# Kernel optimization log

Hardware: AMD Instinct MI355X
Metric: run time of the kernel (lower is better)

Reference implementation:

```python
import jax, jax.numpy as jnp
import numpy as np

HIDDEN = 4096
INTER = 11008
GROUP = 128
B, S = 1, 2048


def setup_inputs() -> dict:
    key = jax.random.key(0)
    ks = jax.random.split(key, 10)
    inp = {
        "x": jax.random.normal(ks[0], (B, S, HIDDEN), dtype=jnp.float32),
        "gate_qw": jax.random.randint(ks[1], (INTER, HIDDEN), 0, 16, dtype=jnp.int32),
        "gate_qz": jax.random.randint(ks[2], (INTER, HIDDEN // GROUP), 0, 16, dtype=jnp.int32),
        "gate_scale": jax.random.uniform(ks[3], (INTER, HIDDEN // GROUP), dtype=jnp.float32) * 0.02,
        "gate_bias": jnp.zeros((INTER,), dtype=jnp.float32),
        "up_qw": jax.random.randint(ks[4], (INTER, HIDDEN), 0, 16, dtype=jnp.int32),
        "up_qz": jax.random.randint(ks[5], (INTER, HIDDEN // GROUP), 0, 16, dtype=jnp.int32),
        "up_scale": jax.random.uniform(ks[6], (INTER, HIDDEN // GROUP), dtype=jnp.float32) * 0.02,
        "up_bias": jnp.zeros((INTER,), dtype=jnp.float32),
        "down_qw": jax.random.randint(ks[7], (HIDDEN, INTER), 0, 16, dtype=jnp.int32),
        "down_qz": jax.random.randint(ks[8], (HIDDEN, INTER // GROUP), 0, 16, dtype=jnp.int32),
        "down_scale": jax.random.uniform(ks[9], (HIDDEN, INTER // GROUP), dtype=jnp.float32) * 0.02,
        "down_bias": jnp.zeros((HIDDEN,), dtype=jnp.float32),
        "group_size": GROUP,
    }
    return inp


def _dequant(qw, qz, scale, group_size):
    # qw: [O, I] int codes in [0,16); qz, scale: [O, I//g]
    O, I = qw.shape
    g = group_size
    q = qw.reshape(O, I // g, g).astype(jnp.float32)
    w = (q - qz[:, :, None].astype(jnp.float32)) * scale[:, :, None]
    return w.reshape(O, I)  # [O, I]


def reference(x, gate_qw, gate_qz, gate_scale, gate_bias,
              up_qw, up_qz, up_scale, up_bias,
              down_qw, down_qz, down_scale, down_bias, group_size):
    Wg = _dequant(gate_qw, gate_qz, gate_scale, group_size)   # [INTER, HIDDEN]
    Wu = _dequant(up_qw, up_qz, up_scale, group_size)         # [INTER, HIDDEN]
    Wd = _dequant(down_qw, down_qz, down_scale, group_size)   # [HIDDEN, INTER]
    g = jnp.einsum('bsh,ih->bsi', x, Wg) + gate_bias          # [B,S,INTER]
    u = jnp.einsum('bsh,ih->bsi', x, Wu) + up_bias            # [B,S,INTER]
    h = jax.nn.silu(g) * u                                    # SwiGLU
    y = jnp.einsum('bsi,hi->bsh', h, Wd) + down_bias          # [B,S,HIDDEN]
    return y
```

## Files before the change

### kernel.cpp

```cpp
#include <hip/hip_runtime.h>
#include <hip/hip_bf16.h>
#include <stdint.h>

#define SEQ    2048
#define HIDDEN 4096
#define INTER  11008

typedef short bf16x8 __attribute__((ext_vector_type(8)));
typedef float f32x4  __attribute__((ext_vector_type(4)));
typedef unsigned short u16x8 __attribute__((ext_vector_type(8)));

#define BAR()  asm volatile("s_barrier" ::: "memory")
#define WAIT6  asm volatile("s_waitcnt vmcnt(6)" ::: "memory")
#define WAIT4  asm volatile("s_waitcnt vmcnt(4)" ::: "memory")
#define WAIT0  asm volatile("s_waitcnt vmcnt(0)" ::: "memory")

__device__ __forceinline__ unsigned short f2bf(float f) {
    union { __hip_bfloat16 h; unsigned short u; } v;
    v.h = __float2bfloat16(f);
    return v.u;
}

__device__ __forceinline__ void gload_lds16(const void* g, void* lds) {
    __builtin_amdgcn_global_load_lds(
        (const __attribute__((address_space(1))) uint32_t*)g,
        (__attribute__((address_space(3))) uint32_t*)lds,
        16, 0, 0);
}

__global__ __launch_bounds__(256) void k_cvt_x(const float* __restrict__ x,
                                               unsigned short* __restrict__ xb) {
    int i = (blockIdx.x * 256 + threadIdx.x) * 4;
    float4 v = *(const float4*)(x + i);
    ushort4 o;
    o.x = f2bf(v.x); o.y = f2bf(v.y); o.z = f2bf(v.z); o.w = f2bf(v.w);
    *(ushort4*)(xb + i) = o;
}

__global__ __launch_bounds__(256) void k_dequant(
    const int* __restrict__ qw, const int* __restrict__ qz,
    const float* __restrict__ sc, unsigned short* __restrict__ w)
{
    size_t i = ((size_t)blockIdx.x * 256 + threadIdx.x) * 8;
    int gi = (int)(i >> 7);
    int   z = qz[gi];
    float s = sc[gi];
    float zs = -(float)z * s;
    int4 q0 = *(const int4*)(qw + i);
    int4 q1 = *(const int4*)(qw + i + 4);
    u16x8 o;
    o[0] = f2bf(fmaf((float)q0.x, s, zs));
    o[1] = f2bf(fmaf((float)q0.y, s, zs));
    o[2] = f2bf(fmaf((float)q0.z, s, zs));
    o[3] = f2bf(fmaf((float)q0.w, s, zs));
    o[4] = f2bf(fmaf((float)q1.x, s, zs));
    o[5] = f2bf(fmaf((float)q1.y, s, zs));
    o[6] = f2bf(fmaf((float)q1.z, s, zs));
    o[7] = f2bf(fmaf((float)q1.w, s, zs));
    *(u16x8*)(w + i) = o;
}

__global__ __launch_bounds__(512) void k_gate_up(
    const unsigned short* __restrict__ xb,
    const unsigned short* __restrict__ wg,
    const unsigned short* __restrict__ wu,
    const float* __restrict__ gbias, const float* __restrict__ ubias,
    unsigned short* __restrict__ h)
{
    __shared__ __align__(16) unsigned short A0[128 * 64], A1[128 * 64];
    __shared__ __align__(16) unsigned short Bg0[128 * 64], Bg1[128 * 64];
    __shared__ __align__(16) unsigned short Bu0[128 * 64], Bu1[128 * 64];

    const int orig = blockIdx.x;
    const int swz  = (orig & 7) * 172 + (orig >> 3);
    const int mt   = swz & 15;
    const int nt   = swz >> 4;
    const int m0   = mt * 128;
    const int n0   = nt * 128;

    const int t    = threadIdx.x;
    const int lane = t & 63;
    const int wave = t >> 6;
    const int wm = (wave >> 2) * 64;
    const int wn = (wave & 3) * 32;

    f32x4 accG[4][2], accU[4][2];
#pragma unroll
    for (int mi = 0; mi < 4; ++mi)
#pragma unroll
        for (int ni = 0; ni < 2; ++ni) {
            accG[mi][ni] = (f32x4){0.f, 0.f, 0.f, 0.f};
            accU[mi][ni] = (f32x4){0.f, 0.f, 0.f, 0.f};
        }

    auto stage = [&](unsigned short* At, unsigned short* Bgt, unsigned short* But,
                     int kt) {
        const int k0 = kt * 64;
#pragma unroll
        for (int cc = 0; cc < 2; ++cc) {
            int idx  = t + 512 * cc;
            int row  = idx >> 3;
            int scol = ((idx & 7) * 16) ^ ((row & 7) << 4);
            gload_lds16((const char*)(xb + (size_t)(m0 + row) * HIDDEN + k0) + scol,
                        (char*)At + idx * 16);
            gload_lds16((const char*)(wg + (size_t)(n0 + row) * HIDDEN + k0) + scol,
                        (char*)Bgt + idx * 16);
            gload_lds16((const char*)(wu + (size_t)(n0 + row) * HIDDEN + k0) + scol,
                        (char*)But + idx * 16);
        }
    };

    auto comp = [&](const unsigned short* At, const unsigned short* Bgt,
                    const unsigned short* But) {
#pragma unroll
        for (int kk = 0; kk < 2; ++kk) {
            bf16x8 af[4], bg[2], bu[2];
#pragma unroll
            for (int mi = 0; mi < 4; ++mi) {
                int row  = wm + mi * 16 + (lane & 15);
                int colb = kk * 64 + ((lane >> 4) * 16);
                af[mi] = *(const bf16x8*)((const char*)At + row * 128 +
                                          (colb ^ ((row & 7) << 4)));
            }
#pragma unroll
            for (int ni = 0; ni < 2; ++ni) {
                int row  = wn + ni * 16 + (lane & 15);
                int colb = kk * 64 + ((lane >> 4) * 16);
                int off  = row * 128 + (colb ^ ((row & 7) << 4));
                bg[ni] = *(const bf16x8*)((const char*)Bgt + off);
                bu[ni] = *(const bf16x8*)((const char*)But + off);
            }
            __builtin_amdgcn_s_setprio(1);
#pragma unroll
            for (int mi = 0; mi < 4; ++mi)
#pragma unroll
                for (int ni = 0; ni < 2; ++ni) {
                    accG[mi][ni] = __builtin_amdgcn_mfma_f32_16x16x32_bf16(
                        af[mi], bg[ni], accG[mi][ni], 0, 0, 0);
                    accU[mi][ni] = __builtin_amdgcn_mfma_f32_16x16x32_bf16(
                        af[mi], bu[ni], accU[mi][ni], 0, 0, 0);
                }
            __builtin_amdgcn_s_setprio(0);
        }
    };

    stage(A0, Bg0, Bu0, 0);
    for (int kt = 0; kt < 62; kt += 2) {
        stage(A1, Bg1, Bu1, kt + 1); WAIT6; BAR(); comp(A0, Bg0, Bu0); BAR();
        stage(A0, Bg0, Bu0, kt + 2); WAIT6; BAR(); comp(A1, Bg1, Bu1); BAR();
    }
    stage(A1, Bg1, Bu1, 63); WAIT6; BAR(); comp(A0, Bg0, Bu0); BAR();
    WAIT0; BAR(); comp(A1, Bg1, Bu1);

#pragma unroll
    for (int ni = 0; ni < 2; ++ni) {
        int col = n0 + wn + ni * 16 + (lane & 15);
        float gb = gbias[col], ub = ubias[col];
#pragma unroll
        for (int mi = 0; mi < 4; ++mi) {
#pragma unroll
            for (int j = 0; j < 4; ++j) {
                int row = m0 + wm + mi * 16 + ((lane >> 4) * 4) + j;
                float g = accG[mi][ni][j] + gb;
                float u = accU[mi][ni][j] + ub;
                float sig = 1.f / (1.f + __expf(-g));
                h[(size_t)row * INTER + col] = f2bf(g * sig * u);
            }
        }
    }
}

__global__ __launch_bounds__(512) void k_down(
    const unsigned short* __restrict__ h,
    const unsigned short* __restrict__ wd,
    const float* __restrict__ dbias,
    float* __restrict__ y)
{
    __shared__ __align__(16) unsigned short A0[128 * 64], A1[128 * 64];
    __shared__ __align__(16) unsigned short B0[128 * 64], B1[128 * 64];

    const int orig = blockIdx.x;
    const int swz  = (orig & 7) * 64 + (orig >> 3);
    const int mt   = swz & 15;
    const int nt   = swz >> 4;
    const int m0   = mt * 128;
    const int n0   = nt * 128;

    const int t    = threadIdx.x;
    const int lane = t & 63;
    const int wave = t >> 6;
    const int wm = (wave >> 2) * 64;
    const int wn = (wave & 3) * 32;

    f32x4 acc[4][2];
#pragma unroll
    for (int mi = 0; mi < 4; ++mi)
#pragma unroll
        for (int ni = 0; ni < 2; ++ni)
            acc[mi][ni] = (f32x4){0.f, 0.f, 0.f, 0.f};

    auto stage = [&](unsigned short* At, unsigned short* Bt, int kt) {
        const int k0 = kt * 64;
#pragma unroll
        for (int cc = 0; cc < 2; ++cc) {
            int idx  = t + 512 * cc;
            int row  = idx >> 3;
            int scol = ((idx & 7) * 16) ^ ((row & 7) << 4);
            gload_lds16((const char*)(h + (size_t)(m0 + row) * INTER + k0) + scol,
                        (char*)At + idx * 16);
            gload_lds16((const char*)(wd + (size_t)(n0 + row) * INTER + k0) + scol,
                        (char*)Bt + idx * 16);
        }
    };

    auto comp = [&](const unsigned short* At, const unsigned short* Bt) {
#pragma unroll
        for (int kk = 0; kk < 2; ++kk) {
            bf16x8 af[4], bd[2];
#pragma unroll
            for (int mi = 0; mi < 4; ++mi) {
                int row  = wm + mi * 16 + (lane & 15);
                int colb = kk * 64 + ((lane >> 4) * 16);
                af[mi] = *(const bf16x8*)((const char*)At + row * 128 +
                                          (colb ^ ((row & 7) << 4)));
            }
#pragma unroll
            for (int ni = 0; ni < 2; ++ni) {
                int row  = wn + ni * 16 + (lane & 15);
                int colb = kk * 64 + ((lane >> 4) * 16);
                bd[ni] = *(const bf16x8*)((const char*)Bt + row * 128 +
                                          (colb ^ ((row & 7) << 4)));
            }
            __builtin_amdgcn_s_setprio(1);
#pragma unroll
            for (int mi = 0; mi < 4; ++mi)
#pragma unroll
                for (int ni = 0; ni < 2; ++ni)
                    acc[mi][ni] = __builtin_amdgcn_mfma_f32_16x16x32_bf16(
                        af[mi], bd[ni], acc[mi][ni], 0, 0, 0);
            __builtin_amdgcn_s_setprio(0);
        }
    };

    stage(A0, B0, 0);
    for (int kt = 0; kt < 170; kt += 2) {
        stage(A1, B1, kt + 1); WAIT4; BAR(); comp(A0, B0); BAR();
        stage(A0, B0, kt + 2); WAIT4; BAR(); comp(A1, B1); BAR();
    }
    stage(A1, B1, 171); WAIT4; BAR(); comp(A0, B0); BAR();
    WAIT0; BAR(); comp(A1, B1);

#pragma unroll
    for (int ni = 0; ni < 2; ++ni) {
        int col = n0 + wn + ni * 16 + (lane & 15);
        float db = dbias[col];
#pragma unroll
        for (int mi = 0; mi < 4; ++mi) {
#pragma unroll
            for (int j = 0; j < 4; ++j) {
                int row = m0 + wm + mi * 16 + ((lane >> 4) * 4) + j;
                y[(size_t)row * HIDDEN + col] = acc[mi][ni][j] + db;
            }
        }
    }
}

extern "C" void kernel_launch(void* const* d_in, const int* in_sizes, int n_in,
                              void* d_out, int out_size, void* d_ws, size_t ws_size,
                              hipStream_t stream) {
    const float* x    = (const float*)d_in[0];
    const int*   gqw  = (const int*)d_in[1];
    const int*   gqz  = (const int*)d_in[2];
    const float* gsc  = (const float*)d_in[3];
    const float* gbia = (const float*)d_in[4];
    const int*   uqw  = (const int*)d_in[5];
    const int*   uqz  = (const int*)d_in[6];
    const float* usc  = (const float*)d_in[7];
    const float* ubia = (const float*)d_in[8];
    const int*   dqw  = (const int*)d_in[9];
    const int*   dqz  = (const int*)d_in[10];
    const float* dsc  = (const float*)d_in[11];
    const float* dbia = (const float*)d_in[12];
    float* y = (float*)d_out;

    const size_t N_XB = (size_t)SEQ * HIDDEN;
    const size_t N_H  = (size_t)SEQ * INTER;
    const size_t N_W  = (size_t)INTER * HIDDEN;

    unsigned short* xb  = (unsigned short*)d_ws;
    unsigned short* hh  = xb + N_XB;
    unsigned short* wgb = hh + N_H;
    unsigned short* wub = wgb + N_W;
    unsigned short* wdb = wgb;

    const int dq_blocks = (int)(N_W / 2048);

    k_cvt_x<<<(SEQ * HIDDEN) / 1024, 256, 0, stream>>>(x, xb);
    k_dequant<<<dq_blocks, 256, 0, stream>>>(gqw, gqz, gsc, wgb);
    k_dequant<<<dq_blocks, 256, 0, stream>>>(uqw, uqz, usc, wub);
    k_gate_up<<<dim3(1376), 512, 0, stream>>>(xb, wgb, wub, gbia, ubia, hh);
    k_dequant<<<dq_blocks, 256, 0, stream>>>(dqw, dqz, dsc, wdb);
    k_down<<<dim3(512), 512, 0, stream>>>(hh, wdb, dbia, y);
}
```

Measured before the change: 848.8 us.

## Enlarge gate/up tile to 256x128, drop double buffering and block swizzle

The gate/up kernel moves from a 128x128 tile to a 256x128 tile with 64x64 per-wave subtiles and twice the accumulators, halving the grid. This cuts repeated weight loads per output. Both GEMM kernels lose their double-buffered LDS pipeline with explicit vmcnt waits and now use a single buffer with __syncthreads around each k-step, so loads no longer overlap compute. The L2-friendly block-index swizzle is also removed, and the larger accumulator set raises register pressure.

```diff
diff --git a/kernel.cpp b/kernel.cpp
--- a/kernel.cpp
+++ b/kernel.cpp
@@ -9,11 +9,6 @@
 typedef short bf16x8 __attribute__((ext_vector_type(8)));
 typedef float f32x4  __attribute__((ext_vector_type(4)));
 typedef unsigned short u16x8 __attribute__((ext_vector_type(8)));
-
-#define BAR()  asm volatile("s_barrier" ::: "memory")
-#define WAIT6  asm volatile("s_waitcnt vmcnt(6)" ::: "memory")
-#define WAIT4  asm volatile("s_waitcnt vmcnt(4)" ::: "memory")
-#define WAIT0  asm volatile("s_waitcnt vmcnt(0)" ::: "memory")
 
 __device__ __forceinline__ unsigned short f2bf(float f) {
     union { __hip_bfloat16 h; unsigned short u; } v;
@@ -67,74 +62,77 @@
     const float* __restrict__ gbias, const float* __restrict__ ubias,
     unsigned short* __restrict__ h)
 {
-    __shared__ __align__(16) unsigned short A0[128 * 64], A1[128 * 64];
-    __shared__ __align__(16) unsigned short Bg0[128 * 64], Bg1[128 * 64];
-    __shared__ __align__(16) unsigned short Bu0[128 * 64], Bu1[128 * 64];
-
-    const int orig = blockIdx.x;
-    const int swz  = (orig & 7) * 172 + (orig >> 3);
-    const int mt   = swz & 15;
-    const int nt   = swz >> 4;
-    const int m0   = mt * 128;
-    const int n0   = nt * 128;
+    __shared__ __align__(16) unsigned short At[256 * 64];
+    __shared__ __align__(16) unsigned short Bg[128 * 64];
+    __shared__ __align__(16) unsigned short Bu[128 * 64];
+
+    const int bid = blockIdx.x;
+    const int mt  = bid & 7;
+    const int nt  = bid >> 3;
+    const int m0  = mt * 256;
+    const int n0  = nt * 128;
 
     const int t    = threadIdx.x;
     const int lane = t & 63;
     const int wave = t >> 6;
-    const int wm = (wave >> 2) * 64;
-    const int wn = (wave & 3) * 32;
-
-    f32x4 accG[4][2], accU[4][2];
+    const int wm = (wave >> 1) * 64;
+    const int wn = (wave & 1) * 64;
+
+    f32x4 accG[4][4], accU[4][4];
 #pragma unroll
     for (int mi = 0; mi < 4; ++mi)
 #pragma unroll
-        for (int ni = 0; ni < 2; ++ni) {
+        for (int ni = 0; ni < 4; ++ni) {
             accG[mi][ni] = (f32x4){0.f, 0.f, 0.f, 0.f};
             accU[mi][ni] = (f32x4){0.f, 0.f, 0.f, 0.f};
         }
 
-    auto stage = [&](unsigned short* At, unsigned short* Bgt, unsigned short* But,
-                     int kt) {
+    for (int kt = 0; kt < HIDDEN / 64; ++kt) {
         const int k0 = kt * 64;
-#pragma unroll
-        for (int cc = 0; cc < 2; ++cc) {
+
+#pragma unroll
+        for (int cc = 0; cc < 4; ++cc) {
             int idx  = t + 512 * cc;
             int row  = idx >> 3;
             int scol = ((idx & 7) * 16) ^ ((row & 7) << 4);
             gload_lds16((const char*)(xb + (size_t)(m0 + row) * HIDDEN + k0) + scol,
                         (char*)At + idx * 16);
+        }
+#pragma unroll
+        for (int cc = 0; cc < 2; ++cc) {
+            int idx  = t + 512 * cc;
+            int row  = idx >> 3;
+            int scol = ((idx & 7) * 16) ^ ((row & 7) << 4);
             gload_lds16((const char*)(wg + (size_t)(n0 + row) * HIDDEN + k0) + scol,
-                        (char*)Bgt + idx * 16);
+                        (char*)Bg + idx * 16);
             gload_lds16((const char*)(wu + (size_t)(n0 + row) * HIDDEN + k0) + scol,
-                        (char*)But + idx * 16);
-        }
-    };
-
-    auto comp = [&](const unsigned short* At, const unsigned short* Bgt,
-                    const unsigned short* But) {
+                        (char*)Bu + idx * 16);
+        }
+
+        __syncthreads();
+
 #pragma unroll
         for (int kk = 0; kk < 2; ++kk) {
-            bf16x8 af[4], bg[2], bu[2];
+            bf16x8 af[4], bg[4], bu[4];
+            int colb = kk * 64 + ((lane >> 4) * 16);
 #pragma unroll
             for (int mi = 0; mi < 4; ++mi) {
-                int row  = wm + mi * 16 + (lane & 15);
-                int colb = kk * 64 + ((lane >> 4) * 16);
+                int row = wm + mi * 16 + (lane & 15);
                 af[mi] = *(const bf16x8*)((const char*)At + row * 128 +
                                           (colb ^ ((row & 7) << 4)));
             }
 #pragma unroll
-            for (int ni = 0; ni < 2; ++ni) {
-                int row  = wn + ni * 16 + (lane & 15);
-                int colb = kk * 64 + ((lane >> 4) * 16);
-                int off  = row * 128 + (colb ^ ((row & 7) << 4));
-                bg[ni] = *(const bf16x8*)((const char*)Bgt + off);
-                bu[ni] = *(const bf16x8*)((const char*)But + off);
+            for (int ni = 0; ni < 4; ++ni) {
+                int row = wn + ni * 16 + (lane & 15);
+                int off = row * 128 + (colb ^ ((row & 7) << 4));
+                bg[ni] = *(const bf16x8*)((const char*)Bg + off);
+                bu[ni] = *(const bf16x8*)((const char*)Bu + off);
             }
             __builtin_amdgcn_s_setprio(1);
 #pragma unroll
             for (int mi = 0; mi < 4; ++mi)
 #pragma unroll
-                for (int ni = 0; ni < 2; ++ni) {
+                for (int ni = 0; ni < 4; ++ni) {
                     accG[mi][ni] = __builtin_amdgcn_mfma_f32_16x16x32_bf16(
                         af[mi], bg[ni], accG[mi][ni], 0, 0, 0);
                     accU[mi][ni] = __builtin_amdgcn_mfma_f32_16x16x32_bf16(
@@ -142,18 +140,12 @@
                 }
             __builtin_amdgcn_s_setprio(0);
         }
-    };
-
-    stage(A0, Bg0, Bu0, 0);
-    for (int kt = 0; kt < 62; kt += 2) {
-        stage(A1, Bg1, Bu1, kt + 1); WAIT6; BAR(); comp(A0, Bg0, Bu0); BAR();
-        stage(A0, Bg0, Bu0, kt + 2); WAIT6; BAR(); comp(A1, Bg1, Bu1); BAR();
-    }
-    stage(A1, Bg1, Bu1, 63); WAIT6; BAR(); comp(A0, Bg0, Bu0); BAR();
-    WAIT0; BAR(); comp(A1, Bg1, Bu1);
-
-#pragma unroll
-    for (int ni = 0; ni < 2; ++ni) {
+
+        __syncthreads();
+    }
+
+#pragma unroll
+    for (int ni = 0; ni < 4; ++ni) {
         int col = n0 + wn + ni * 16 + (lane & 15);
         float gb = gbias[col], ub = ubias[col];
 #pragma unroll
@@ -176,15 +168,14 @@
     const float* __restrict__ dbias,
     float* __restrict__ y)
 {
-    __shared__ __align__(16) unsigned short A0[128 * 64], A1[128 * 64];
-    __shared__ __align__(16) unsigned short B0[128 * 64], B1[128 * 64];
-
-    const int orig = blockIdx.x;
-    const int swz  = (orig & 7) * 64 + (orig >> 3);
-    const int mt   = swz & 15;
-    const int nt   = swz >> 4;
-    const int m0   = mt * 128;
-    const int n0   = nt * 128;
+    __shared__ __align__(16) unsigned short At[128 * 64];
+    __shared__ __align__(16) unsigned short Bd[128 * 64];
+
+    const int bid = blockIdx.x;
+    const int mt  = bid & 15;
+    const int nt  = bid >> 4;
+    const int m0  = mt * 128;
+    const int n0  = nt * 128;
 
     const int t    = threadIdx.x;
     const int lane = t & 63;
@@ -199,8 +190,9 @@
         for (int ni = 0; ni < 2; ++ni)
             acc[mi][ni] = (f32x4){0.f, 0.f, 0.f, 0.f};
 
-    auto stage = [&](unsigned short* At, unsigned short* Bt, int kt) {
+    for (int kt = 0; kt < INTER / 64; ++kt) {
         const int k0 = kt * 64;
+
 #pragma unroll
         for (int cc = 0; cc < 2; ++cc) {
             int idx  = t + 512 * cc;
@@ -209,11 +201,11 @@
             gload_lds16((const char*)(h + (size_t)(m0 + row) * INTER + k0) + scol,
                         (char*)At + idx * 16);
             gload_lds16((const char*)(wd + (size_t)(n0 + row) * INTER + k0) + scol,
-                        (char*)Bt + idx * 16);
-        }
-    };
-
-    auto comp = [&](const unsigned short* At, const unsigned short* Bt) {
+                        (char*)Bd + idx * 16);
+        }
+
+        __syncthreads();
+
 #pragma unroll
         for (int kk = 0; kk < 2; ++kk) {
             bf16x8 af[4], bd[2];
@@ -228,7 +220,7 @@
             for (int ni = 0; ni < 2; ++ni) {
                 int row  = wn + ni * 16 + (lane & 15);
                 int colb = kk * 64 + ((lane >> 4) * 16);
-                bd[ni] = *(const bf16x8*)((const char*)Bt + row * 128 +
+                bd[ni] = *(const bf16x8*)((const char*)Bd + row * 128 +
                                           (colb ^ ((row & 7) << 4)));
             }
             __builtin_amdgcn_s_setprio(1);
@@ -240,15 +232,9 @@
                         af[mi], bd[ni], acc[mi][ni], 0, 0, 0);
             __builtin_amdgcn_s_setprio(0);
         }
-    };
-
-    stage(A0, B0, 0);
-    for (int kt = 0; kt < 170; kt += 2) {
-        stage(A1, B1, kt + 1); WAIT4; BAR(); comp(A0, B0); BAR();
-        stage(A0, B0, kt + 2); WAIT4; BAR(); comp(A1, B1); BAR();
-    }
-    stage(A1, B1, 171); WAIT4; BAR(); comp(A0, B0); BAR();
-    WAIT0; BAR(); comp(A1, B1);
+
+        __syncthreads();
+    }
 
 #pragma unroll
     for (int ni = 0; ni < 2; ++ni) {
@@ -298,7 +284,7 @@
     k_cvt_x<<<(SEQ * HIDDEN) / 1024, 256, 0, stream>>>(x, xb);
     k_dequant<<<dq_blocks, 256, 0, stream>>>(gqw, gqz, gsc, wgb);
     k_dequant<<<dq_blocks, 256, 0, stream>>>(uqw, uqz, usc, wub);
-    k_gate_up<<<dim3(1376), 512, 0, stream>>>(xb, wgb, wub, gbia, ubia, hh);
+    k_gate_up<<<dim3(688), 512, 0, stream>>>(xb, wgb, wub, gbia, ubia, hh);
     k_dequant<<<dq_blocks, 256, 0, stream>>>(dqw, dqz, dsc, wdb);
     k_down<<<dim3(512), 512, 0, stream>>>(hh, wdb, dbia, y);
 }
```

Result: no change. 845.9 us (-0.3%).

## Switch GEMM pipelines to triple-buffered 32-wide K stages with new LDS swizzle

Applied to the files above, without the earlier changes.

Both the gate/up and down GEMMs now stage 32-element K slices into three rotating LDS buffers instead of 64-element slices into two. Each thread issues one 16-byte direct-to-LDS load per operand per stage, using a new row-pair swizzle for the stores and a matching fragment read pattern. This keeps two stages of global loads in flight ahead of compute, and the total LDS footprint per block shrinks. The cost is twice as many barriers and wait points, with half as many MFMAs between each pair.

```diff
diff --git a/kernel.cpp b/kernel.cpp
--- a/kernel.cpp
+++ b/kernel.cpp
@@ -11,9 +11,11 @@
 typedef unsigned short u16x8 __attribute__((ext_vector_type(8)));
 
 #define BAR()  asm volatile("s_barrier" ::: "memory")
-#define WAIT6  asm volatile("s_waitcnt vmcnt(6)" ::: "memory")
-#define WAIT4  asm volatile("s_waitcnt vmcnt(4)" ::: "memory")
-#define WAIT0  asm volatile("s_waitcnt vmcnt(0)" ::: "memory")
+#define W6()   asm volatile("s_waitcnt vmcnt(6)" ::: "memory")
+#define W4()   asm volatile("s_waitcnt vmcnt(4)" ::: "memory")
+#define W3()   asm volatile("s_waitcnt vmcnt(3)" ::: "memory")
+#define W2()   asm volatile("s_waitcnt vmcnt(2)" ::: "memory")
+#define W0()   asm volatile("s_waitcnt vmcnt(0)" ::: "memory")
 
 __device__ __forceinline__ unsigned short f2bf(float f) {
     union { __hip_bfloat16 h; unsigned short u; } v;
@@ -60,6 +62,7 @@
     *(u16x8*)(w + i) = o;
 }
 
+
 __global__ __launch_bounds__(512) void k_gate_up(
     const unsigned short* __restrict__ xb,
     const unsigned short* __restrict__ wg,
@@ -67,9 +70,9 @@
     const float* __restrict__ gbias, const float* __restrict__ ubias,
     unsigned short* __restrict__ h)
 {
-    __shared__ __align__(16) unsigned short A0[128 * 64], A1[128 * 64];
-    __shared__ __align__(16) unsigned short Bg0[128 * 64], Bg1[128 * 64];
-    __shared__ __align__(16) unsigned short Bu0[128 * 64], Bu1[128 * 64];
+    __shared__ __align__(16) unsigned short A_[3][128 * 32];
+    __shared__ __align__(16) unsigned short Bg_[3][128 * 32];
+    __shared__ __align__(16) unsigned short Bu_[3][128 * 32];
 
     const int orig = blockIdx.x;
     const int swz  = (orig & 7) * 172 + (orig >> 3);
@@ -84,6 +87,14 @@
     const int wm = (wave >> 2) * 64;
     const int wn = (wave & 3) * 32;
 
+    const int srow = t >> 3;
+    const int sl   = (t & 7) ^ (srow & 7);
+    const int lrow = srow * 2 + (sl >> 2);
+    const int lcolb = (sl & 3) * 16;
+
+    const int sS   = ((((lane & 1) << 2) | (lane >> 4)) ^ ((lane >> 1) & 7)) * 16;
+    const int lrh  = (lane & 15) >> 1;
+
     f32x4 accG[4][2], accU[4][2];
 #pragma unroll
     for (int mi = 0; mi < 4; ++mi)
@@ -93,64 +104,50 @@
             accU[mi][ni] = (f32x4){0.f, 0.f, 0.f, 0.f};
         }
 
-    auto stage = [&](unsigned short* At, unsigned short* Bgt, unsigned short* But,
-                     int kt) {
-        const int k0 = kt * 64;
-#pragma unroll
-        for (int cc = 0; cc < 2; ++cc) {
-            int idx  = t + 512 * cc;
-            int row  = idx >> 3;
-            int scol = ((idx & 7) * 16) ^ ((row & 7) << 4);
-            gload_lds16((const char*)(xb + (size_t)(m0 + row) * HIDDEN + k0) + scol,
-                        (char*)At + idx * 16);
-            gload_lds16((const char*)(wg + (size_t)(n0 + row) * HIDDEN + k0) + scol,
-                        (char*)Bgt + idx * 16);
-            gload_lds16((const char*)(wu + (size_t)(n0 + row) * HIDDEN + k0) + scol,
-                        (char*)But + idx * 16);
-        }
-    };
-
-    auto comp = [&](const unsigned short* At, const unsigned short* Bgt,
-                    const unsigned short* But) {
-#pragma unroll
-        for (int kk = 0; kk < 2; ++kk) {
-            bf16x8 af[4], bg[2], bu[2];
-#pragma unroll
-            for (int mi = 0; mi < 4; ++mi) {
-                int row  = wm + mi * 16 + (lane & 15);
-                int colb = kk * 64 + ((lane >> 4) * 16);
-                af[mi] = *(const bf16x8*)((const char*)At + row * 128 +
-                                          (colb ^ ((row & 7) << 4)));
+    auto stage = [&](int buf, int ph) {
+        const int k0 = ph * 32;
+        const char* xs = (const char*)(xb + (size_t)(m0 + lrow) * HIDDEN + k0) + lcolb;
+        const char* gs = (const char*)(wg + (size_t)(n0 + lrow) * HIDDEN + k0) + lcolb;
+        const char* us = (const char*)(wu + (size_t)(n0 + lrow) * HIDDEN + k0) + lcolb;
+        gload_lds16(xs, (char*)A_[buf]  + t * 16);
+        gload_lds16(gs, (char*)Bg_[buf] + t * 16);
+        gload_lds16(us, (char*)Bu_[buf] + t * 16);
+    };
+
+    auto comp = [&](int buf) {
+        bf16x8 af[4], bg[2], bu[2];
+#pragma unroll
+        for (int mi = 0; mi < 4; ++mi)
+            af[mi] = *(const bf16x8*)((const char*)A_[buf] +
+                        (wm / 2 + mi * 8 + lrh) * 128 + sS);
+#pragma unroll
+        for (int ni = 0; ni < 2; ++ni) {
+            int off = (wn / 2 + ni * 8 + lrh) * 128 + sS;
+            bg[ni] = *(const bf16x8*)((const char*)Bg_[buf] + off);
+            bu[ni] = *(const bf16x8*)((const char*)Bu_[buf] + off);
+        }
+        __builtin_amdgcn_s_setprio(1);
+#pragma unroll
+        for (int mi = 0; mi < 4; ++mi)
+#pragma unroll
+            for (int ni = 0; ni < 2; ++ni) {
+                accG[mi][ni] = __builtin_amdgcn_mfma_f32_16x16x32_bf16(
+                    af[mi], bg[ni], accG[mi][ni], 0, 0, 0);
+                accU[mi][ni] = __builtin_amdgcn_mfma_f32_16x16x32_bf16(
+                    af[mi], bu[ni], accU[mi][ni], 0, 0, 0);
             }
-#pragma unroll
-            for (int ni = 0; ni < 2; ++ni) {
-                int row  = wn + ni * 16 + (lane & 15);
-                int colb = kk * 64 + ((lane >> 4) * 16);
-                int off  = row * 128 + (colb ^ ((row & 7) << 4));
-                bg[ni] = *(const bf16x8*)((const char*)Bgt + off);
-                bu[ni] = *(const bf16x8*)((const char*)But + off);
-            }
-            __builtin_amdgcn_s_setprio(1);
-#pragma unroll
-            for (int mi = 0; mi < 4; ++mi)
-#pragma unroll
-                for (int ni = 0; ni < 2; ++ni) {
-                    accG[mi][ni] = __builtin_amdgcn_mfma_f32_16x16x32_bf16(
-                        af[mi], bg[ni], accG[mi][ni], 0, 0, 0);
-                    accU[mi][ni] = __builtin_amdgcn_mfma_f32_16x16x32_bf16(
-                        af[mi], bu[ni], accU[mi][ni], 0, 0, 0);
-                }
-            __builtin_amdgcn_s_setprio(0);
-        }
-    };
-
-    stage(A0, Bg0, Bu0, 0);
-    for (int kt = 0; kt < 62; kt += 2) {
-        stage(A1, Bg1, Bu1, kt + 1); WAIT6; BAR(); comp(A0, Bg0, Bu0); BAR();
-        stage(A0, Bg0, Bu0, kt + 2); WAIT6; BAR(); comp(A1, Bg1, Bu1); BAR();
-    }
-    stage(A1, Bg1, Bu1, 63); WAIT6; BAR(); comp(A0, Bg0, Bu0); BAR();
-    WAIT0; BAR(); comp(A1, Bg1, Bu1);
+        __builtin_amdgcn_s_setprio(0);
+    };
+
+    stage(0, 0);
+    stage(1, 1);
+    for (int ph = 0; ph + 4 < 128; ph += 3) {
+        stage(2, ph + 2); W6(); BAR(); comp(0); BAR();
+        stage(0, ph + 3); W6(); BAR(); comp(1); BAR();
+        stage(1, ph + 4); W6(); BAR(); comp(2); BAR();
+    }
+    W3(); BAR(); comp(0);
+    W0(); BAR(); comp(1);
 
 #pragma unroll
     for (int ni = 0; ni < 2; ++ni) {
@@ -176,8 +173,8 @@
     const float* __restrict__ dbias,
     float* __restrict__ y)
 {
-    __shared__ __align__(16) unsigned short A0[128 * 64], A1[128 * 64];
-    __shared__ __align__(16) unsigned short B0[128 * 64], B1[128 * 64];
+    __shared__ __align__(16) unsigned short A_[3][128 * 32];
+    __shared__ __align__(16) unsigned short B_[3][128 * 32];
 
     const int orig = blockIdx.x;
     const int swz  = (orig & 7) * 64 + (orig >> 3);
@@ -192,6 +189,14 @@
     const int wm = (wave >> 2) * 64;
     const int wn = (wave & 3) * 32;
 
+    const int srow = t >> 3;
+    const int sl   = (t & 7) ^ (srow & 7);
+    const int lrow = srow * 2 + (sl >> 2);
+    const int lcolb = (sl & 3) * 16;
+
+    const int sS   = ((((lane & 1) << 2) | (lane >> 4)) ^ ((lane >> 1) & 7)) * 16;
+    const int lrh  = (lane & 15) >> 1;
+
     f32x4 acc[4][2];
 #pragma unroll
     for (int mi = 0; mi < 4; ++mi)
@@ -199,56 +204,43 @@
         for (int ni = 0; ni < 2; ++ni)
             acc[mi][ni] = (f32x4){0.f, 0.f, 0.f, 0.f};
 
-    auto stage = [&](unsigned short* At, unsigned short* Bt, int kt) {
-        const int k0 = kt * 64;
-#pragma unroll
-        for (int cc = 0; cc < 2; ++cc) {
-            int idx  = t + 512 * cc;
-            int row  = idx >> 3;
-            int scol = ((idx & 7) * 16) ^ ((row & 7) << 4);
-            gload_lds16((const char*)(h + (size_t)(m0 + row) * INTER + k0) + scol,
-                        (char*)At + idx * 16);
-            gload_lds16((const char*)(wd + (size_t)(n0 + row) * INTER + k0) + scol,
-                        (char*)Bt + idx * 16);
-        }
-    };
-
-    auto comp = [&](const unsigned short* At, const unsigned short* Bt) {
-#pragma unroll
-        for (int kk = 0; kk < 2; ++kk) {
-            bf16x8 af[4], bd[2];
-#pragma unroll
-            for (int mi = 0; mi < 4; ++mi) {
-                int row  = wm + mi * 16 + (lane & 15);
-                int colb = kk * 64 + ((lane >> 4) * 16);
-                af[mi] = *(const bf16x8*)((const char*)At + row * 128 +
-                                          (colb ^ ((row & 7) << 4)));
-            }
-#pragma unroll
-            for (int ni = 0; ni < 2; ++ni) {
-                int row  = wn + ni * 16 + (lane & 15);
-                int colb = kk * 64 + ((lane >> 4) * 16);
-                bd[ni] = *(const bf16x8*)((const char*)Bt + row * 128 +
-                                          (colb ^ ((row & 7) << 4)));
-            }
-            __builtin_amdgcn_s_setprio(1);
-#pragma unroll
-            for (int mi = 0; mi < 4; ++mi)
-#pragma unroll
-                for (int ni = 0; ni < 2; ++ni)
-                    acc[mi][ni] = __builtin_amdgcn_mfma_f32_16x16x32_bf16(
-                        af[mi], bd[ni], acc[mi][ni], 0, 0, 0);
-            __builtin_amdgcn_s_setprio(0);
-        }
-    };
-
-    stage(A0, B0, 0);
-    for (int kt = 0; kt < 170; kt += 2) {
-        stage(A1, B1, kt + 1); WAIT4; BAR(); comp(A0, B0); BAR();
-        stage(A0, B0, kt + 2); WAIT4; BAR(); comp(A1, B1); BAR();
-    }
-    stage(A1, B1, 171); WAIT4; BAR(); comp(A0, B0); BAR();
-    WAIT0; BAR(); comp(A1, B1);
+    auto stage = [&](int buf, int ph) {
+        const int k0 = ph * 32;
+        gload_lds16((const char*)(h  + (size_t)(m0 + lrow) * INTER + k0) + lcolb,
+                    (char*)A_[buf] + t * 16);
+        gload_lds16((const char*)(wd + (size_t)(n0 + lrow) * INTER + k0) + lcolb,
+                    (char*)B_[buf] + t * 16);
+    };
+
+    auto comp = [&](int buf) {
+        bf16x8 af[4], bd[2];
+#pragma unroll
+        for (int mi = 0; mi < 4; ++mi)
+            af[mi] = *(const bf16x8*)((const char*)A_[buf] +
+                        (wm / 2 + mi * 8 + lrh) * 128 + sS);
+#pragma unroll
+        for (int ni = 0; ni < 2; ++ni)
+            bd[ni] = *(const bf16x8*)((const char*)B_[buf] +
+                        (wn / 2 + ni * 8 + lrh) * 128 + sS);
+        __builtin_amdgcn_s_setprio(1);
+#pragma unroll
+        for (int mi = 0; mi < 4; ++mi)
+#pragma unroll
+            for (int ni = 0; ni < 2; ++ni)
+                acc[mi][ni] = __builtin_amdgcn_mfma_f32_16x16x32_bf16(
+                    af[mi], bd[ni], acc[mi][ni], 0, 0, 0);
+        __builtin_amdgcn_s_setprio(0);
+    };
+
+    stage(0, 0);
+    stage(1, 1);
+    for (int ph = 0; ph + 4 < 344; ph += 3) {
+        stage(2, ph + 2); W4(); BAR(); comp(0); BAR();
+        stage(0, ph + 3); W4(); BAR(); comp(1); BAR();
+        stage(1, ph + 4); W4(); BAR(); comp(2); BAR();
+    }
+    W2(); BAR(); comp(0);
+    W0(); BAR(); comp(1);
 
 #pragma unroll
     for (int ni = 0; ni < 2; ++ni) {
```

Result: slower. 1.005 ms (+18.4%).
